# Performance work log

Measured on AMD Instinct MI355X. Metric: run time of the kernel, lower is better.

The kernel has to match this reference:

```python
import jax, jax.numpy as jnp
import numpy as np

B, S, D, H = 2, 2048, 2048, 16
HD = D // H  # head dim = 128


def setup_inputs() -> dict:
    key = jax.random.key(0)
    ks = jax.random.split(key, 9)
    sc = 1.0 / np.sqrt(D)
    return {
        "hidden_states": jax.random.normal(ks[0], (B, S, D), jnp.float32),
        "Wq": jax.random.normal(ks[1], (D, D), jnp.float32) * sc,
        "bq": jax.random.normal(ks[2], (D,), jnp.float32) * 0.02,
        "Wk": jax.random.normal(ks[3], (D, D), jnp.float32) * sc,
        "bk": jax.random.normal(ks[4], (D,), jnp.float32) * 0.02,
        "Wv": jax.random.normal(ks[5], (D, D), jnp.float32) * sc,
        "bv": jax.random.normal(ks[6], (D,), jnp.float32) * 0.02,
        "Wo": jax.random.normal(ks[7], (D, D), jnp.float32) * sc,
        "bo": jax.random.normal(ks[8], (D,), jnp.float32) * 0.02,
    }


def _rotate_half(x):
    x1, x2 = jnp.split(x, 2, axis=-1)
    return jnp.concatenate((-x2, x1), axis=-1)


def reference(hidden_states, Wq, bq, Wk, bk, Wv, bv, Wo, bo):
    b, s, d = hidden_states.shape
    # QKV projections (torch Linear: x @ W.T + b)
    def proj(W, bias):
        y = jnp.einsum('bsd,ed->bse', hidden_states, W) + bias
        return y.reshape(b, s, H, HD).transpose(0, 2, 1, 3)  # [B,H,S,HD]
    q, k, v = proj(Wq, bq), proj(Wk, bk), proj(Wv, bv)

    # Rotary embedding tables
    inv_freq = 1.0 / (10000.0 ** (jnp.arange(0, HD, 2, dtype=jnp.float32) / HD))
    t = jnp.arange(s, dtype=jnp.float32)
    freqs = jnp.einsum('i,j->ij', t, inv_freq)          # [S, HD/2]
    emb = jnp.concatenate((freqs, freqs), axis=-1)       # [S, HD]
    cos_cached, sin_cached = jnp.cos(emb), jnp.sin(emb)
    # NOTE: source unpacks `sin, cos = rotary_emb(...)` while forward returns
    # (cos, sin) -> swap is intentional to match original math.
    sin_t, cos_t = cos_cached, sin_cached
    q = q * cos_t + _rotate_half(q) * sin_t
    k = k * cos_t + _rotate_half(k) * sin_t

    scores = jnp.einsum('bhsd,bhtd->bhst', q, k) / jnp.sqrt(jnp.float32(HD))
    probs = jax.nn.softmax(scores, axis=-1)
    ctx = jnp.einsum('bhst,bhtd->bhsd', probs, v)
    ctx = ctx.transpose(0, 2, 1, 3).reshape(b, s, d)
    return jnp.einsum('bsd,ed->bse', ctx, Wo) + bo
```

## Files before the change

### kernel.cpp

```cpp
#include <hip/hip_runtime.h>

constexpr int NH = 16;
constexpr int SEQ = 2048;
constexpr int DMODEL = 2048;
constexpr int HDIM = 128;
constexpr int NB = 2;
constexpr int MTOT = NB * SEQ;
constexpr long NEL = (long)NB * SEQ * DMODEL;
constexpr long WEL = (long)DMODEL * DMODEL;
constexpr size_t FUSED_WS = 2ul * (4 * NEL + 3 * WEL + 12288);

typedef __attribute__((ext_vector_type(8))) __bf16 bf16x8;
typedef __attribute__((ext_vector_type(4))) float f32x4;

__device__ __forceinline__ float bf2f(ushort u) {
  union { uint i; float f; } v; v.i = ((uint)u) << 16; return v.f;
}
__device__ __forceinline__ ushort f2bf(float f) {
  union { float f; uint i; } v; v.f = f;
  uint r = (v.i + 0x7FFFu + ((v.i >> 16) & 1u)) >> 16;
  return (ushort)r;
}
__device__ __forceinline__ ushort f2bf_rhu(float f) {
  union { float f; uint i; } v; v.f = f;
  return (ushort)((v.i + 0x8000u) >> 16);
}
__device__ __forceinline__ float fast_exp2(float x) {
#if __has_builtin(__builtin_amdgcn_exp2f)
  return __builtin_amdgcn_exp2f(x);
#else
  float r;
  asm volatile("v_exp_f32 %0, %1\n\ts_nop 0" : "=v"(r) : "v"(x));
  return r;
#endif
}

__global__ __launch_bounds__(256) void conv_f32_bf16(
    const float* __restrict__ s, ushort* __restrict__ d, int n4) {
  const int i = blockIdx.x * 256 + threadIdx.x;
  if (i < n4) {
    const float4 v = ((const float4*)s)[i];
    ushort4 o;
    o.x = f2bf(v.x); o.y = f2bf(v.y); o.z = f2bf(v.z); o.w = f2bf(v.w);
    ((ushort4*)d)[i] = o;
  }
}

__global__ __launch_bounds__(256) void bias_cat(
    const float* __restrict__ a, const float* __restrict__ b,
    const float* __restrict__ c, float* __restrict__ o) {
  const int i = blockIdx.x * 256 + threadIdx.x;
  o[i] = (i < 2048) ? a[i] : (i < 4096) ? b[i - 2048] : c[i - 4096];
}

#define GLDS(src, dst)                                              \
  __builtin_amdgcn_global_load_lds(                                 \
      (const __attribute__((address_space(1))) void*)(src),         \
      (__attribute__((address_space(3))) void*)(dst), 16, 0, 0)

#define STAGE_A(d, mh, kc) do {                                     \
    const ushort* _s = gA + (long)((mh) * 128) * K + (kc) * 64;     \
    ushort* _d = smem + (d) * 16384 + (mh) * 8192 + w * 1024;       \
    GLDS(_s, _d);                                                   \
    GLDS(_s + 8 * (long)K, _d + 512);                               \
  } while (0)

#define STAGE_B(d, nh, kc) do {                                     \
    const ushort* _s = gB + (long)((nh) * 128) * K + (kc) * 64;     \
    ushort* _d = smem + 32768 + (d) * 16384 + (nh) * 8192 + w * 1024; \
    GLDS(_s, _d);                                                   \
    GLDS(_s + 8 * (long)K, _d + 512);                               \
  } while (0)

#define LDA(d, mh) do {                                             \
    const ushort* _p = smem + (d) * 16384 + (mh) * 8192 +           \
                       (wm * 64 + l16) * 64;                        \
    _Pragma("unroll")                                               \
    for (int _i = 0; _i < 4; _i++) {                                \
      afr[_i][0] = *(const bf16x8*)(_p + _i * 1024 + sw0);          \
      afr[_i][1] = *(const bf16x8*)(_p + _i * 1024 + sw1);          \
    }                                                               \
  } while (0)

#define LDB(d, nh) do {                                             \
    const ushort* _p = smem + 32768 + (d) * 16384 + (nh) * 8192 +   \
                       (wn * 32 + l16) * 64;                        \
    _Pragma("unroll")                                               \
    for (int _j = 0; _j < 2; _j++) {                                \
      bfr[nh][_j][0] = *(const bf16x8*)(_p + _j * 1024 + sw0);      \
      bfr[nh][_j][1] = *(const bf16x8*)(_p + _j * 1024 + sw1);      \
    }                                                               \
  } while (0)

#define MMA(mh, nh) do {                                            \
    __builtin_amdgcn_s_setprio(1);                                  \
    _Pragma("unroll")                                               \
    for (int _i = 0; _i < 4; _i++)                                  \
      _Pragma("unroll")                                             \
      for (int _j = 0; _j < 2; _j++) {                              \
        acc[mh][_i][nh][_j] = __builtin_amdgcn_mfma_f32_16x16x32_bf16( \
            afr[_i][0], bfr[nh][_j][0], acc[mh][_i][nh][_j], 0, 0, 0); \
        acc[mh][_i][nh][_j] = __builtin_amdgcn_mfma_f32_16x16x32_bf16( \
            afr[_i][1], bfr[nh][_j][1], acc[mh][_i][nh][_j], 0, 0, 0); \
      }                                                             \
    __builtin_amdgcn_s_setprio(0);                                  \
  } while (0)

#define BARX() __builtin_amdgcn_s_barrier()
#define WAITV(n) asm volatile("s_waitcnt vmcnt(" #n ")" ::: "memory")
#define WAITL() asm volatile("s_waitcnt lgkmcnt(0)" ::: "memory")

template <int MODE>
__global__ __launch_bounds__(512, 2) void gemm256(
    const ushort* __restrict__ A, const ushort* __restrict__ Bw,
    const float* __restrict__ bias, void* __restrict__ Cv,
    int M, int N, int K) {
  __shared__ __align__(16) ushort smem[65536];
  const int tid = threadIdx.x;
  const int w = tid >> 6, lane = tid & 63;
  const int quad = lane >> 4, l16 = lane & 15;
  const int wm = w >> 2, wn = w & 3;
  const int nbm = M >> 8, nbn = N >> 8;
  const int rm = nbm >> 1, rn = nbn >> 2;
  const int xcd = blockIdx.x & 7, loc = blockIdx.x >> 3;
  const int bm = (xcd >> 2) * rm + (loc % rm);
  const int bn = (xcd & 3) * rn + (loc / rm);
  const int m0 = bm << 8, n0 = bn << 8;
  const int KT = K >> 6;

  const int srow = (w << 4) + (lane >> 3);
  const int scol = ((lane & 7) ^ (lane >> 3)) << 3;
  const ushort* gA = A + (long)(m0 + srow) * K + scol;
  const ushort* gB = Bw + (long)(n0 + srow) * K + scol;
  const int sw0 = ((quad ^ (lane & 7)) << 3);
  const int sw1 = (((4 + quad) ^ (lane & 7)) << 3);

  f32x4 acc[2][4][2][2] = {};
  bf16x8 afr[4][2];
  bf16x8 bfr[2][2][2];

  STAGE_A(0, 0, 0); STAGE_B(0, 0, 0); STAGE_B(0, 1, 0); STAGE_A(0, 1, 0);
  STAGE_A(1, 0, 1); STAGE_B(1, 0, 1);
  WAITV(4);
  BARX();

  for (int t = 0; t < KT; t += 2) {
    const int c2 = (t + 2 < KT) ? t + 2 : 0;
    const int c3 = (t + 3 < KT) ? t + 3 : (t + 3 - KT);
    STAGE_B(1, 1, t + 1); WAITV(6); BARX();
    LDA(0, 0); LDB(0, 0); WAITL();
    MMA(0, 0); BARX();
    LDB(0, 1); STAGE_A(1, 1, t + 1); BARX(); WAITL();
    MMA(0, 1); BARX();
    LDA(0, 1); STAGE_A(0, 0, c2); BARX(); WAITL();
    MMA(1, 0); BARX();
    STAGE_B(0, 0, c2); BARX();
    MMA(1, 1); BARX();
    STAGE_B(0, 1, c2); WAITV(6); BARX();
    LDA(1, 0); LDB(1, 0); WAITL();
    MMA(0, 0); BARX();
    LDB(1, 1); STAGE_A(0, 1, c2); BARX(); WAITL();
    MMA(0, 1); BARX();
    LDA(1, 1); STAGE_A(1, 0, c3); BARX(); WAITL();
    MMA(1, 0); BARX();
    STAGE_B(1, 0, c3); BARX();
    MMA(1, 1); BARX();
  }

#pragma unroll
  for (int mh = 0; mh < 2; mh++)
#pragma unroll
    for (int i = 0; i < 4; i++) {
      const int rbase = m0 + mh * 128 + wm * 64 + i * 16 + quad * 4;
#pragma unroll
      for (int nh = 0; nh < 2; nh++)
#pragma unroll
        for (int j = 0; j < 2; j++) {
          const int col = n0 + nh * 128 + wn * 32 + j * 16 + l16;
          const float bv = bias[col];
#pragma unroll
          for (int r = 0; r < 4; r++) {
            const int row = rbase + r;
            const float v = acc[mh][i][nh][j][r] + bv;
            if (MODE == 0) {
              ((float*)Cv)[(long)row * N + col] = v;
            } else {
              const int b = row >> 11, s = row & (SEQ - 1);
              const int h = (col >> 7) & 15, hd = col & (HDIM - 1);
              const long off = (long)(col >> 11) * NEL +
                  ((long)(b * NH + h) * SEQ + s) * HDIM + hd;
              ((ushort*)Cv)[off] = f2bf(v);
            }
          }
        }
    }
}

__global__ __launch_bounds__(256) void rope_qk(ushort* Q, ushort* Kt) {
  const int gid = blockIdx.x * 256 + threadIdx.x;
  const int n = gid & 4194303;
  const bool isK = (gid >= 4194304);
  ushort* ptr = isK ? Kt : Q;
  const float qs = isK ? 1.0f : 0.12751743f;
  const int p = n & 63;
  const int s = (n >> 6) & (SEQ - 1);
  const int bh = n >> 17;
  const long idx = (long)bh * (SEQ * HDIM) + (long)s * HDIM + p;
  const float invf_rev =
      fast_exp2(-(float)p * 0.2076205059304601f) * 0.15915494309189535f;
  float rev = (float)s * invf_rev;
  rev -= floorf(rev);
  const float sn = __builtin_amdgcn_sinf(rev);
  const float cs = __builtin_amdgcn_cosf(rev);
  const float x1 = bf2f(ptr[idx]);
  const float x2 = bf2f(ptr[idx + 64]);
  ptr[idx]      = f2bf((x1 * sn - x2 * cs) * qs);
  ptr[idx + 64] = f2bf((x2 * sn + x1 * cs) * qs);
}

__global__ __launch_bounds__(256) void transpose_v(const ushort* __restrict__ V,
                                                   ushort* __restrict__ VT) {
  __shared__ ushort lT[64 * 65];
  const int bh = blockIdx.x >> 6;
  const int rem = blockIdx.x & 63;
  const int t0 = (rem >> 1) << 6, d0 = (rem & 1) << 6;
  const ushort* vb = V + (long)bh * (SEQ * HDIM);
  ushort* ob = VT + (long)bh * (SEQ * HDIM);
  const int tid = threadIdx.x;
#pragma unroll
  for (int it = 0; it < 16; it++) {
    const int idx = it * 256 + tid;
    const int r = idx >> 6, c = idx & 63;
    lT[c * 65 + r] = vb[(long)(t0 + r) * HDIM + d0 + c];
  }
  __syncthreads();
#pragma unroll
  for (int it = 0; it < 16; it++) {
    const int idx = it * 256 + tid;
    const int r = idx >> 6, c = idx & 63;
    ob[(long)(d0 + r) * SEQ + t0 + c] = lT[r * 65 + c];
  }
}

__global__ __launch_bounds__(256, 2) void attn(const ushort* __restrict__ Q,
                                               const ushort* __restrict__ Kp,
                                               const ushort* __restrict__ VT,
                                               ushort* __restrict__ ctx) {
  __shared__ __align__(16) ushort smem[40960];
  const int tid = threadIdx.x;
  const int wave = tid >> 6, lane = tid & 63;
  const int quad = lane >> 4, l16 = lane & 15;
  const int xcd = blockIdx.x & 7, loc = blockIdx.x >> 3;
  const int bh = xcd * 4 + (loc >> 5), qt = loc & 31;
  const long hb = (long)bh * (SEQ * HDIM);
  const int b = bh >> 4, h = bh & 15;
  const int qh = wave & 1, th = wave >> 1;
  ushort* myP = smem + 35840 + wave * (32 * 40);

  bf16x8 qa[2][4];
#pragma unroll
  for (int qq = 0; qq < 2; qq++)
#pragma unroll
    for (int c = 0; c < 4; c++)
      qa[qq][c] = *(const bf16x8*)(
          Q + hb + (long)(qt * 64 + qh * 32 + qq * 16 + l16) * HDIM +
          c * 32 + (quad << 3));

  f32x4 o[2][8] = {};
  f32x4 lacc[2] = {};
  bf16x8 ones;
#pragma unroll
  for (int i = 0; i < 8; i++) ones[i] = (__bf16)1.0f;

  const ushort* kSrc = Kp + hb + (long)(tid >> 4) * HDIM + (tid & 15) * 8;
  const ushort* vSrc = VT + hb + (long)(tid >> 3) * SEQ + (tid & 7) * 8;
  const int kOff = (tid >> 4) * 136 + (tid & 15) * 8;
  const int vOff = (tid >> 3) * 72 + (tid & 7) * 8;

  {
    bf16x8 kR[4], vR[4];
#pragma unroll
    for (int it = 0; it < 4; it++) {
      kR[it] = *(const bf16x8*)(kSrc + (long)it * (16 * HDIM));
      vR[it] = *(const bf16x8*)(vSrc + (long)it * (32 * SEQ));
    }
    kSrc += 64 * HDIM; vSrc += 64;
#pragma unroll
    for (int it = 0; it < 4; it++) {
      *(bf16x8*)(smem + kOff + it * (16 * 136)) = kR[it];
      *(bf16x8*)(smem + 17408 + vOff + it * (32 * 72)) = vR[it];
    }
  }
  __syncthreads();

  for (int t0 = 0; t0 < SEQ; t0 += 64) {
    const int cur = (t0 >> 6) & 1;
    ushort* cK = cur ? smem + 8704 : smem;
    ushort* cV = cur ? smem + 26624 : smem + 17408;
    ushort* nK = cur ? smem : smem + 8704;
    ushort* nV = cur ? smem + 17408 : smem + 26624;
    const bool more = (t0 + 64 < SEQ);

    bf16x8 kR[4], vR[4];
    if (more) {
#pragma unroll
      for (int it = 0; it < 4; it++) {
        kR[it] = *(const bf16x8*)(kSrc + (long)it * (16 * HDIM));
        vR[it] = *(const bf16x8*)(vSrc + (long)it * (32 * SEQ));
      }
      kSrc += 64 * HDIM; vSrc += 64;
    }

    const ushort* kRow = cK + (th * 32 + l16) * 136 + (quad << 3);
    f32x4 st[2][2] = {};
    __builtin_amdgcn_s_setprio(1);
#pragma unroll
    for (int kc = 0; kc < 4; kc++)
#pragma unroll
      for (int tt = 0; tt < 2; tt++) {
        const bf16x8 ka = *(const bf16x8*)(kRow + tt * (16 * 136) + kc * 32);
#pragma unroll
        for (int qq = 0; qq < 2; qq++)
          st[tt][qq] = __builtin_amdgcn_mfma_f32_16x16x32_bf16(
              ka, qa[qq][kc], st[tt][qq], 0, 0, 0);
      }
    __builtin_amdgcn_s_setprio(0);

    ushort* pW = myP + l16 * 40 + (quad << 2);
#pragma unroll
    for (int qq = 0; qq < 2; qq++)
#pragma unroll
      for (int tt = 0; tt < 2; tt++) {
        ushort4 pk;
        pk.x = f2bf_rhu(fast_exp2(st[tt][qq][0]));
        pk.y = f2bf_rhu(fast_exp2(st[tt][qq][1]));
        pk.z = f2bf_rhu(fast_exp2(st[tt][qq][2]));
        pk.w = f2bf_rhu(fast_exp2(st[tt][qq][3]));
        *(ushort4*)(pW + qq * (16 * 40) + tt * 16) = pk;
      }
    WAITL();
    __builtin_amdgcn_sched_barrier(0);

    const ushort* pRow = myP + l16 * 40 + (quad << 3);
    const ushort* vRow = cV + l16 * 72 + th * 32 + (quad << 3);
    bf16x8 pa[2];
    __builtin_amdgcn_s_setprio(1);
#pragma unroll
    for (int qq = 0; qq < 2; qq++) {
      pa[qq] = *(const bf16x8*)(pRow + qq * (16 * 40));
      lacc[qq] = __builtin_amdgcn_mfma_f32_16x16x32_bf16(
          pa[qq], ones, lacc[qq], 0, 0, 0);
    }
#pragma unroll
    for (int nt = 0; nt < 8; nt++) {
      const bf16x8 vb = *(const bf16x8*)(vRow + nt * (16 * 72));
#pragma unroll
      for (int qq = 0; qq < 2; qq++)
        o[qq][nt] = __builtin_amdgcn_mfma_f32_16x16x32_bf16(
            pa[qq], vb, o[qq][nt], 0, 0, 0);
    }
    __builtin_amdgcn_s_setprio(0);

    if (more) {
#pragma unroll
      for (int it = 0; it < 4; it++) {
        *(bf16x8*)(nK + kOff + it * (16 * 136)) = kR[it];
        *(bf16x8*)(nV + vOff + it * (32 * 72)) = vR[it];
      }
    }
    __syncthreads();
  }

  float* mb = (float*)smem;
  if (wave >= 2) {
    float* p = mb + ((wave - 2) * 64 + lane) * 73;
#pragma unroll
    for (int qq = 0; qq < 2; qq++) {
#pragma unroll
      for (int nt = 0; nt < 8; nt++)
#pragma unroll
        for (int r = 0; r < 4; r++) p[qq * 32 + nt * 4 + r] = o[qq][nt][r];
#pragma unroll
      for (int r = 0; r < 4; r++) p[64 + qq * 4 + r] = lacc[qq][r];
    }
  }
  __syncthreads();
  if (wave < 2) {
    const float* p = mb + (wave * 64 + lane) * 73;
#pragma unroll
    for (int qq = 0; qq < 2; qq++) {
#pragma unroll
      for (int nt = 0; nt < 8; nt++)
#pragma unroll
        for (int r = 0; r < 4; r++) o[qq][nt][r] += p[qq * 32 + nt * 4 + r];
#pragma unroll
      for (int r = 0; r < 4; r++) lacc[qq][r] += p[64 + qq * 4 + r];
    }
#pragma unroll
    for (int qq = 0; qq < 2; qq++)
#pragma unroll
      for (int r = 0; r < 4; r++) {
        const float inv = 1.0f / lacc[qq][r];
        const int s = qt * 64 + qh * 32 + qq * 16 + quad * 4 + r;
        const long base = ((long)(b * SEQ + s)) * DMODEL + h * HDIM;
#pragma unroll
        for (int nt = 0; nt < 8; nt++)
          ctx[base + nt * 16 + l16] = f2bf(o[qq][nt][r] * inv);
      }
  }
}

extern "C" void kernel_launch(void* const* d_in, const int* in_sizes, int n_in,
                              void* d_out, int out_size, void* d_ws, size_t ws_size,
                              hipStream_t stream) {
  const float* hid = (const float*)d_in[0];
  const float* Wq = (const float*)d_in[1];
  const float* bq = (const float*)d_in[2];
  const float* Wk = (const float*)d_in[3];
  const float* bk = (const float*)d_in[4];
  const float* Wv = (const float*)d_in[5];
  const float* bv = (const float*)d_in[6];
  const float* Wo = (const float*)d_in[7];
  const float* bo = (const float*)d_in[8];
  float* out = (float*)d_out;
  ushort* ws = (ushort*)d_ws;

  ushort* qw   = ws;
  ushort* kw   = ws + NEL;
  ushort* vw   = ws + 2 * NEL;
  ushort* hidB = ws + 3 * NEL;
  ushort* wB   = ws + 4 * NEL;

  dim3 blk(256);
  dim3 blkG(512);
  conv_f32_bf16<<<(int)(NEL / 4 / 256), blk, 0, stream>>>(hid, hidB, NEL / 4);

  if (ws_size >= FUSED_WS) {
    conv_f32_bf16<<<(int)(WEL / 4 / 256), blk, 0, stream>>>(Wq, wB, WEL / 4);
    conv_f32_bf16<<<(int)(WEL / 4 / 256), blk, 0, stream>>>(Wk, wB + WEL, WEL / 4);
    conv_f32_bf16<<<(int)(WEL / 4 / 256), blk, 0, stream>>>(Wv, wB + 2 * WEL, WEL / 4);
    float* bc = (float*)(wB + 3 * WEL);
    bias_cat<<<24, blk, 0, stream>>>(bq, bk, bv, bc);
    gemm256<1><<<384, blkG, 0, stream>>>(hidB, wB, bc, qw, MTOT, 3 * DMODEL, DMODEL);
  } else {
    conv_f32_bf16<<<(int)(WEL / 4 / 256), blk, 0, stream>>>(Wq, wB, WEL / 4);
    gemm256<1><<<128, blkG, 0, stream>>>(hidB, wB, bq, qw, MTOT, DMODEL, DMODEL);
    conv_f32_bf16<<<(int)(WEL / 4 / 256), blk, 0, stream>>>(Wk, wB, WEL / 4);
    gemm256<1><<<128, blkG, 0, stream>>>(hidB, wB, bk, kw, MTOT, DMODEL, DMODEL);
    conv_f32_bf16<<<(int)(WEL / 4 / 256), blk, 0, stream>>>(Wv, wB, WEL / 4);
    gemm256<1><<<128, blkG, 0, stream>>>(hidB, wB, bv, vw, MTOT, DMODEL, DMODEL);
  }

  rope_qk<<<32768, blk, 0, stream>>>(qw, kw);

  ushort* vtw = hidB;
  transpose_v<<<2048, blk, 0, stream>>>(vw, vtw);

  ushort* cw = vw;
  attn<<<1024, blk, 0, stream>>>(qw, kw, vtw, cw);

  conv_f32_bf16<<<(int)(WEL / 4 / 256), blk, 0, stream>>>(Wo, wB, WEL / 4);
  gemm256<0><<<128, blkG, 0, stream>>>(cw, wB, bo, out, MTOT, DMODEL, DMODEL);
}
```

Measured before the change: 431.4 us.

## Shrink GEMM tile to 128x256 with a new single-K-step pipeline

Replaces the 256x256 GEMM tile with a 128x256 tile, which halves the accumulator registers and cuts LDS use from 128KB to 96KB. The staging and MMA schedule is rewritten as a per-K-step double buffer for A and B. This doubles the grid size: 768 blocks for the fused QKV GEMM and 256 for the output projection, giving better CU occupancy and wave balance on a 256-CU part. The trade-off is lower arithmetic intensity per block and more global and L2 traffic for B.

Measured after the change: 423.1 us. Within noise of the previous version (-1.9%).

```diff
diff --git a/kernel.cpp b/kernel.cpp
--- a/kernel.cpp
+++ b/kernel.cpp
@@ -58,23 +58,29 @@
       (const __attribute__((address_space(1))) void*)(src),         \
       (__attribute__((address_space(3))) void*)(dst), 16, 0, 0)
 
-#define STAGE_A(d, mh, kc) do {                                     \
-    const ushort* _s = gA + (long)((mh) * 128) * K + (kc) * 64;     \
-    ushort* _d = smem + (d) * 16384 + (mh) * 8192 + w * 1024;       \
+#define STG_A(d, kt) do {                                           \
+    const ushort* _s = gA + (long)(kt) * 64;                        \
+    ushort* _d = smem + (d) * 8192 + w * 512;                       \
     GLDS(_s, _d);                                                   \
-    GLDS(_s + 8 * (long)K, _d + 512);                               \
-  } while (0)
-
-#define STAGE_B(d, nh, kc) do {                                     \
-    const ushort* _s = gB + (long)((nh) * 128) * K + (kc) * 64;     \
-    ushort* _d = smem + 32768 + (d) * 16384 + (nh) * 8192 + w * 1024; \
+    GLDS(_s + 64 * (long)K, _d + 4096);                             \
+  } while (0)
+
+#define STG_B0(d, kt) do {                                          \
+    const ushort* _s = gB + (long)(kt) * 64;                        \
+    ushort* _d = smem + 16384 + (d) * 16384 + w * 512;              \
     GLDS(_s, _d);                                                   \
-    GLDS(_s + 8 * (long)K, _d + 512);                               \
-  } while (0)
-
-#define LDA(d, mh) do {                                             \
-    const ushort* _p = smem + (d) * 16384 + (mh) * 8192 +           \
-                       (wm * 64 + l16) * 64;                        \
+    GLDS(_s + 64 * (long)K, _d + 4096);                             \
+  } while (0)
+
+#define STG_B1(d, kt) do {                                          \
+    const ushort* _s = gB + 128 * (long)K + (long)(kt) * 64;        \
+    ushort* _d = smem + 16384 + (d) * 16384 + 8192 + w * 512;       \
+    GLDS(_s, _d);                                                   \
+    GLDS(_s + 64 * (long)K, _d + 4096);                             \
+  } while (0)
+
+#define LDAF(d) do {                                                \
+    const ushort* _p = smem + (d) * 8192 + (wm * 64 + l16) * 64;    \
     _Pragma("unroll")                                               \
     for (int _i = 0; _i < 4; _i++) {                                \
       afr[_i][0] = *(const bf16x8*)(_p + _i * 1024 + sw0);          \
@@ -82,9 +88,9 @@
     }                                                               \
   } while (0)
 
-#define LDB(d, nh) do {                                             \
-    const ushort* _p = smem + 32768 + (d) * 16384 + (nh) * 8192 +   \
-                       (wn * 32 + l16) * 64;                        \
+#define LDBF(d, nh) do {                                            \
+    const ushort* _p = smem + 16384 + (d) * 16384 +                 \
+                       ((nh) * 128 + wn * 32 + l16) * 64;           \
     _Pragma("unroll")                                               \
     for (int _j = 0; _j < 2; _j++) {                                \
       bfr[nh][_j][0] = *(const bf16x8*)(_p + _j * 1024 + sw0);      \
@@ -92,16 +98,16 @@
     }                                                               \
   } while (0)
 
-#define MMA(mh, nh) do {                                            \
+#define MMAP(nh) do {                                               \
     __builtin_amdgcn_s_setprio(1);                                  \
     _Pragma("unroll")                                               \
     for (int _i = 0; _i < 4; _i++)                                  \
       _Pragma("unroll")                                             \
       for (int _j = 0; _j < 2; _j++) {                              \
-        acc[mh][_i][nh][_j] = __builtin_amdgcn_mfma_f32_16x16x32_bf16( \
-            afr[_i][0], bfr[nh][_j][0], acc[mh][_i][nh][_j], 0, 0, 0); \
-        acc[mh][_i][nh][_j] = __builtin_amdgcn_mfma_f32_16x16x32_bf16( \
-            afr[_i][1], bfr[nh][_j][1], acc[mh][_i][nh][_j], 0, 0, 0); \
+        acc[_i][(nh) * 2 + _j] = __builtin_amdgcn_mfma_f32_16x16x32_bf16( \
+            afr[_i][0], bfr[nh][_j][0], acc[_i][(nh) * 2 + _j], 0, 0, 0); \
+        acc[_i][(nh) * 2 + _j] = __builtin_amdgcn_mfma_f32_16x16x32_bf16( \
+            afr[_i][1], bfr[nh][_j][1], acc[_i][(nh) * 2 + _j], 0, 0, 0); \
       }                                                             \
     __builtin_amdgcn_s_setprio(0);                                  \
   } while (0)
@@ -111,89 +117,89 @@
 #define WAITL() asm volatile("s_waitcnt lgkmcnt(0)" ::: "memory")
 
 template <int MODE>
-__global__ __launch_bounds__(512, 2) void gemm256(
+__global__ __launch_bounds__(512, 2) void gemm128(
     const ushort* __restrict__ A, const ushort* __restrict__ Bw,
     const float* __restrict__ bias, void* __restrict__ Cv,
     int M, int N, int K) {
-  __shared__ __align__(16) ushort smem[65536];
+  __shared__ __align__(16) ushort smem[49152];
   const int tid = threadIdx.x;
   const int w = tid >> 6, lane = tid & 63;
   const int quad = lane >> 4, l16 = lane & 15;
   const int wm = w >> 2, wn = w & 3;
-  const int nbm = M >> 8, nbn = N >> 8;
+  const int nbm = M >> 7, nbn = N >> 8;
   const int rm = nbm >> 1, rn = nbn >> 2;
   const int xcd = blockIdx.x & 7, loc = blockIdx.x >> 3;
   const int bm = (xcd >> 2) * rm + (loc % rm);
   const int bn = (xcd & 3) * rn + (loc / rm);
-  const int m0 = bm << 8, n0 = bn << 8;
+  const int m0 = bm << 7, n0 = bn << 8;
   const int KT = K >> 6;
 
-  const int srow = (w << 4) + (lane >> 3);
-  const int scol = ((lane & 7) ^ (lane >> 3)) << 3;
+  const int srow = tid >> 3;
+  const int scol = (((tid & 7) ^ ((tid >> 3) & 7)) << 3);
   const ushort* gA = A + (long)(m0 + srow) * K + scol;
   const ushort* gB = Bw + (long)(n0 + srow) * K + scol;
-  const int sw0 = ((quad ^ (lane & 7)) << 3);
-  const int sw1 = (((4 + quad) ^ (lane & 7)) << 3);
-
-  f32x4 acc[2][4][2][2] = {};
+  const int sw0 = ((quad ^ (l16 & 7)) << 3);
+  const int sw1 = (((4 + quad) ^ (l16 & 7)) << 3);
+
+  f32x4 acc[4][4] = {};
   bf16x8 afr[4][2];
   bf16x8 bfr[2][2][2];
 
-  STAGE_A(0, 0, 0); STAGE_B(0, 0, 0); STAGE_B(0, 1, 0); STAGE_A(0, 1, 0);
-  STAGE_A(1, 0, 1); STAGE_B(1, 0, 1);
+  STG_B1(0, 0);
+  STG_A(0, 0); STG_B0(0, 0);
+  STG_A(1, 1); STG_B0(1, 1);
   WAITV(4);
   BARX();
-
-  for (int t = 0; t < KT; t += 2) {
-    const int c2 = (t + 2 < KT) ? t + 2 : 0;
-    const int c3 = (t + 3 < KT) ? t + 3 : (t + 3 - KT);
-    STAGE_B(1, 1, t + 1); WAITV(6); BARX();
-    LDA(0, 0); LDB(0, 0); WAITL();
-    MMA(0, 0); BARX();
-    LDB(0, 1); STAGE_A(1, 1, t + 1); BARX(); WAITL();
-    MMA(0, 1); BARX();
-    LDA(0, 1); STAGE_A(0, 0, c2); BARX(); WAITL();
-    MMA(1, 0); BARX();
-    STAGE_B(0, 0, c2); BARX();
-    MMA(1, 1); BARX();
-    STAGE_B(0, 1, c2); WAITV(6); BARX();
-    LDA(1, 0); LDB(1, 0); WAITL();
-    MMA(0, 0); BARX();
-    LDB(1, 1); STAGE_A(0, 1, c2); BARX(); WAITL();
-    MMA(0, 1); BARX();
-    LDA(1, 1); STAGE_A(1, 0, c3); BARX(); WAITL();
-    MMA(1, 0); BARX();
-    STAGE_B(1, 0, c3); BARX();
-    MMA(1, 1); BARX();
-  }
-
-#pragma unroll
-  for (int mh = 0; mh < 2; mh++)
-#pragma unroll
-    for (int i = 0; i < 4; i++) {
-      const int rbase = m0 + mh * 128 + wm * 64 + i * 16 + quad * 4;
-#pragma unroll
-      for (int nh = 0; nh < 2; nh++)
-#pragma unroll
-        for (int j = 0; j < 2; j++) {
-          const int col = n0 + nh * 128 + wn * 32 + j * 16 + l16;
-          const float bv = bias[col];
-#pragma unroll
-          for (int r = 0; r < 4; r++) {
-            const int row = rbase + r;
-            const float v = acc[mh][i][nh][j][r] + bv;
-            if (MODE == 0) {
-              ((float*)Cv)[(long)row * N + col] = v;
-            } else {
-              const int b = row >> 11, s = row & (SEQ - 1);
-              const int h = (col >> 7) & 15, hd = col & (HDIM - 1);
-              const long off = (long)(col >> 11) * NEL +
-                  ((long)(b * NH + h) * SEQ + s) * HDIM + hd;
-              ((ushort*)Cv)[off] = f2bf(v);
-            }
+  LDAF(0); LDBF(0, 0);
+  WAITL();
+  BARX();
+
+  for (int t = 0; t < KT; t++) {
+    const int d = t & 1, nd = d ^ 1;
+    const int c1 = (t + 1 < KT) ? t + 1 : 0;
+    const int c2 = (t + 2 < KT) ? t + 2 : (t + 2 - KT);
+    STG_B1(nd, c1);
+    STG_A(d, c2);
+    WAITV(8);
+    BARX();
+    WAITL();
+    MMAP(0);
+    LDBF(d, 1);
+    BARX();
+    STG_B0(d, c2);
+    WAITV(6);
+    BARX();
+    WAITL();
+    MMAP(1);
+    LDAF(nd); LDBF(nd, 0);
+    BARX();
+  }
+
+#pragma unroll
+  for (int i = 0; i < 4; i++) {
+    const int rbase = m0 + wm * 64 + i * 16 + quad * 4;
+#pragma unroll
+    for (int nh = 0; nh < 2; nh++)
+#pragma unroll
+      for (int j = 0; j < 2; j++) {
+        const int col = n0 + nh * 128 + wn * 32 + j * 16 + l16;
+        const float bv = bias[col];
+#pragma unroll
+        for (int r = 0; r < 4; r++) {
+          const int row = rbase + r;
+          const float v = acc[i][nh * 2 + j][r] + bv;
+          if (MODE == 0) {
+            ((float*)Cv)[(long)row * N + col] = v;
+          } else {
+            const int b = row >> 11, s = row & (SEQ - 1);
+            const int h = (col >> 7) & 15, hd = col & (HDIM - 1);
+            const long off = (long)(col >> 11) * NEL +
+                ((long)(b * NH + h) * SEQ + s) * HDIM + hd;
+            ((ushort*)Cv)[off] = f2bf(v);
           }
         }
-    }
+      }
+  }
 }
 
 __global__ __launch_bounds__(256) void rope_qk(ushort* Q, ushort* Kt) {
@@ -441,14 +447,14 @@
     conv_f32_bf16<<<(int)(WEL / 4 / 256), blk, 0, stream>>>(Wv, wB + 2 * WEL, WEL / 4);
     float* bc = (float*)(wB + 3 * WEL);
     bias_cat<<<24, blk, 0, stream>>>(bq, bk, bv, bc);
-    gemm256<1><<<384, blkG, 0, stream>>>(hidB, wB, bc, qw, MTOT, 3 * DMODEL, DMODEL);
+    gemm128<1><<<768, blkG, 0, stream>>>(hidB, wB, bc, qw, MTOT, 3 * DMODEL, DMODEL);
   } else {
     conv_f32_bf16<<<(int)(WEL / 4 / 256), blk, 0, stream>>>(Wq, wB, WEL / 4);
-    gemm256<1><<<128, blkG, 0, stream>>>(hidB, wB, bq, qw, MTOT, DMODEL, DMODEL);
+    gemm128<1><<<256, blkG, 0, stream>>>(hidB, wB, bq, qw, MTOT, DMODEL, DMODEL);
     conv_f32_bf16<<<(int)(WEL / 4 / 256), blk, 0, stream>>>(Wk, wB, WEL / 4);
-    gemm256<1><<<128, blkG, 0, stream>>>(hidB, wB, bk, kw, MTOT, DMODEL, DMODEL);
+    gemm128<1><<<256, blkG, 0, stream>>>(hidB, wB, bk, kw, MTOT, DMODEL, DMODEL);
     conv_f32_bf16<<<(int)(WEL / 4 / 256), blk, 0, stream>>>(Wv, wB, WEL / 4);
-    gemm256<1><<<128, blkG, 0, stream>>>(hidB, wB, bv, vw, MTOT, DMODEL, DMODEL);
+    gemm128<1><<<256, blkG, 0, stream>>>(hidB, wB, bv, vw, MTOT, DMODEL, DMODEL);
   }
 
   rope_qk<<<32768, blk, 0, stream>>>(qw, kw);
@@ -460,5 +466,5 @@
   attn<<<1024, blk, 0, stream>>>(qw, kw, vtw, cw);
 
   conv_f32_bf16<<<(int)(WEL / 4 / 256), blk, 0, stream>>>(Wo, wB, WEL / 4);
-  gemm256<0><<<128, blkG, 0, stream>>>(cw, wB, bo, out, MTOT, DMODEL, DMODEL);
-}
+  gemm128<0><<<256, blkG, 0, stream>>>(cw, wB, bo, out, MTOT, DMODEL, DMODEL);
+}
```
